# Kernel tuning notes

Hardware: AMD Instinct MI355X
Metric: run time of the kernel (lower is better)

The kernel has to match this reference:

```python
import jax, jax.numpy as jnp
import numpy as np

NUM_HEAD = 16
EMBD_DIM = 2048
LATENT_DIM = 512
ROPE_DIM = 64  # min(rope_dim, head_dim) = 64
HEAD_DIM = EMBD_DIM // NUM_HEAD  # 128
ROPE_HALF = ROPE_DIM // 2
SCALE = (HEAD_DIM + ROPE_DIM) ** -0.5


def setup_inputs() -> dict:
    key = jax.random.key(0)
    ks = jax.random.split(key, 9)
    B, S = 2, 2048
    std = 0.02
    return {
        "x": jax.random.normal(ks[0], (B, S, EMBD_DIM), dtype=jnp.float32),
        "w_ckv": jax.random.normal(ks[1], (EMBD_DIM, LATENT_DIM), dtype=jnp.float32) * std,
        "w_k": jax.random.normal(ks[2], (LATENT_DIM, EMBD_DIM), dtype=jnp.float32) * std,
        "w_v": jax.random.normal(ks[3], (LATENT_DIM, EMBD_DIM), dtype=jnp.float32) * std,
        "w_cq": jax.random.normal(ks[4], (EMBD_DIM, LATENT_DIM), dtype=jnp.float32) * std,
        "w_q": jax.random.normal(ks[5], (LATENT_DIM, EMBD_DIM), dtype=jnp.float32) * std,
        "w_qr": jax.random.normal(ks[6], (LATENT_DIM, NUM_HEAD * ROPE_DIM), dtype=jnp.float32) * std,
        "w_kr": jax.random.normal(ks[7], (EMBD_DIM, ROPE_DIM), dtype=jnp.float32) * std,
        "w_o": jax.random.normal(ks[8], (EMBD_DIM, EMBD_DIM), dtype=jnp.float32) * std,
    }


def _apply_rope(x, S):
    # x: [B, H, S, D] with D >= ROPE_DIM; interleaved even/odd rotation
    inv_freq = 1.0 / (10000.0 ** (jnp.arange(0, ROPE_DIM, 2, dtype=jnp.float32) / ROPE_DIM))
    pos = jnp.arange(S, dtype=jnp.float32)
    freqs = pos[:, None] * inv_freq[None, :]           # [S, ROPE_HALF]
    cos = jnp.cos(freqs)[None, None]                   # [1,1,S,ROPE_HALF]
    sin = jnp.sin(freqs)[None, None]
    x_rope, x_pass = x[..., :ROPE_DIM], x[..., ROPE_DIM:]
    x_even, x_odd = x_rope[..., 0::2], x_rope[..., 1::2]
    r_even = x_even * cos - x_odd * sin
    r_odd = x_even * sin + x_odd * cos
    rotated = jnp.stack([r_even, r_odd], axis=-1).reshape(x_rope.shape)
    return jnp.concatenate([rotated, x_pass], axis=-1) if x_pass.shape[-1] > 0 else rotated


def reference(x, w_ckv, w_k, w_v, w_cq, w_q, w_qr, w_kr, w_o):
    B, S, _ = x.shape
    c_kv = x @ w_ckv                                   # [B,S,latent]
    k_c = (c_kv @ w_k).reshape(B, S, NUM_HEAD, HEAD_DIM).transpose(0, 2, 1, 3)
    v = (c_kv @ w_v).reshape(B, S, NUM_HEAD, HEAD_DIM).transpose(0, 2, 1, 3)
    c_q = x @ w_cq
    q_c = (c_q @ w_q).reshape(B, S, NUM_HEAD, HEAD_DIM).transpose(0, 2, 1, 3)
    q_r = (c_q @ w_qr).reshape(B, S, NUM_HEAD, ROPE_DIM).transpose(0, 2, 1, 3)
    k_r = (x @ w_kr)[:, None, :, :]                    # [B,1,S,rope] shared across heads
    k_r = jnp.broadcast_to(k_r, (B, NUM_HEAD, S, ROPE_DIM))
    q_r = _apply_rope(q_r, S)
    k_r = _apply_rope(k_r, S)
    q = jnp.concatenate([q_c, q_r], axis=-1)           # [B,H,S,head+rope]
    k = jnp.concatenate([k_c, k_r], axis=-1)
    scores = jnp.einsum("bhsd,bhtd->bhst", q, k) * SCALE
    causal = jnp.tril(jnp.ones((S, S), dtype=bool))
    scores = jnp.where(causal[None, None], scores, -jnp.inf)
    attn = jax.nn.softmax(scores, axis=-1)
    out = jnp.einsum("bhst,bhtd->bhsd", attn, v)       # [B,H,S,head]
    out = out.transpose(0, 2, 1, 3).reshape(B, S, EMBD_DIM)
    return out @ w_o
```

## Files before the change

kernel.cpp:

```cpp
#include <hip/hip_runtime.h>


typedef unsigned short u16;
typedef __attribute__((ext_vector_type(8))) short s16x8;
typedef __attribute__((ext_vector_type(4))) float f32x4;
typedef __attribute__((ext_vector_type(8))) __bf16 bf16x8;
typedef __attribute__((ext_vector_type(4))) u16 u16x4;

#define S_LEN 2048
#define NH 16
#define HD 128
#define DQK 192
#define EMB 2048

#define GLOAD_LDS16(g, l)                                                      \
  __builtin_amdgcn_global_load_lds(                                            \
      (const __attribute__((address_space(1))) unsigned int*)(g),              \
      (__attribute__((address_space(3))) unsigned int*)(l), 16, 0, 0)

__device__ __forceinline__ u16 f2b(float f) {
  unsigned u = __builtin_bit_cast(unsigned, f);
  u += 0x7FFFu + ((u >> 16) & 1u);
  return (u16)(u >> 16);
}
__device__ __forceinline__ float b2f(u16 v) {
  unsigned u = ((unsigned)v) << 16;
  return __builtin_bit_cast(float, u);
}
__device__ __forceinline__ bf16x8 ld_bf8(const u16* p) {
  return __builtin_bit_cast(bf16x8, *(const s16x8*)p);
}

__device__ __forceinline__ void transpose_tile(const float* __restrict__ in,
                                               u16* __restrict__ out,
                                               int K, int N, int local, int t,
                                               u16* T ) {
  int nt = N >> 6;
  int n0 = (local % nt) * 64, k0 = (local / nt) * 64;
#pragma unroll
  for (int r = 0; r < 4; ++r) {
    int kl = (t >> 4) + r * 16, nl = (t & 15) * 4;
    f32x4 v = *(const f32x4*)(in + (size_t)(k0 + kl) * N + n0 + nl);
#pragma unroll
    for (int j = 0; j < 4; ++j) T[(nl + j) * 72 + kl] = f2b(v[j]);
  }
  __syncthreads();
#pragma unroll
  for (int r = 0; r < 2; ++r) {
    int chunk = t + r * 256, nr = chunk >> 3, kc = (chunk & 7) * 8;
    *(s16x8*)(out + (size_t)(n0 + nr) * K + k0 + kc) = *(const s16x8*)(&T[nr * 72 + kc]);
  }
}

__global__ __launch_bounds__(256) void prep_kernel(
    const float* __restrict__ xf, u16* __restrict__ XB,
    const float* __restrict__ wckvf, u16* __restrict__ WCKV_T,
    const float* __restrict__ wcqf,  u16* __restrict__ WCQ_T,
    const float* __restrict__ wkrf,  u16* __restrict__ WKR_T,
    const float* __restrict__ wkf,   u16* __restrict__ WK_T,
    const float* __restrict__ wvf,   u16* __restrict__ WV_T,
    const float* __restrict__ wqf,   u16* __restrict__ WQ_T,
    const float* __restrict__ wqrf,  u16* __restrict__ WQR_T,
    const float* __restrict__ wof,   u16* __restrict__ WO_T,
    float* __restrict__ cosT, float* __restrict__ sinT) {
  __shared__ u16 T[64 * 72];
  const int id = blockIdx.x, t = threadIdx.x;
  if (id < 8192) {
    int i = id * 256 + t;
    f32x4 v = *(const f32x4*)(xf + (size_t)i * 4);
    u16x4 o = { f2b(v[0]), f2b(v[1]), f2b(v[2]), f2b(v[3]) };
    *(u16x4*)(XB + (size_t)i * 4) = o;
  } else if (id < 8448)  { transpose_tile(wckvf, WCKV_T, 2048, 512,  id - 8192, t, T); }
  else if (id < 8704)    { transpose_tile(wcqf,  WCQ_T,  2048, 512,  id - 8448, t, T); }
  else if (id < 8736)    { transpose_tile(wkrf,  WKR_T,  2048, 64,   id - 8704, t, T); }
  else if (id < 8992)    { transpose_tile(wkf,   WK_T,   512,  2048, id - 8736, t, T); }
  else if (id < 9248)    { transpose_tile(wvf,   WV_T,   512,  2048, id - 8992, t, T); }
  else if (id < 9504)    { transpose_tile(wqf,   WQ_T,   512,  2048, id - 9248, t, T); }
  else if (id < 9632)    { transpose_tile(wqrf,  WQR_T,  512,  1024, id - 9504, t, T); }
  else if (id < 10656)   { transpose_tile(wof,   WO_T,   2048, 2048, id - 9632, t, T); }
  else {
    int i2 = (id - 10656) * 256 + t;
    int s = i2 >> 5, i = i2 & 31;
    float inv = exp2f(-(float)i * (13.287712379549449f / 32.0f));
    float ang = (float)s * inv;
    cosT[i2] = cosf(ang);
    sinT[i2] = sinf(ang);
  }
}

template<int MODE>
__global__ __launch_bounds__(256) void gemm_bt_kernel(const u16* __restrict__ A,
                                                      int lda,
                                                      const u16* __restrict__ BT,
                                                      void* __restrict__ C0,
                                                      void* __restrict__ C1,
                                                      void* __restrict__ C2,
                                                      void* __restrict__ C3,
                                                      int M, int N, int K,
                                                      int nx, float scale) {
  __shared__ __align__(16) u16 As[2][128 * 64];
  __shared__ __align__(16) u16 Bs[2][128 * 64];
  const int t = threadIdx.x;
  const int lane = t & 63, wid = t >> 6;
  const int wr = (wid >> 1) * 64, wc = (wid & 1) * 64;
  const int cpx = gridDim.x >> 3;
  int wg = blockIdx.x;
  wg = (wg & 7) * cpx + (wg >> 3);
  const int bn0 = (wg % nx) * 128;
  const int bm0 = (wg / nx) * 128;
  if (MODE == 6 && bn0 >= 4096) A += 512;
  const int lr = lane & 15, lg = lane >> 4;

  auto stage = [&](int k0, int buf) {
#pragma unroll
    for (int r = 0; r < 4; ++r) {
      int chunk = t + r * 256;
      int row = chunk >> 3, kcs = (chunk & 7) * 8;
      int kcg = kcs ^ ((row & 7) << 3);
      GLOAD_LDS16(A + (size_t)(bm0 + row) * lda + k0 + kcg, &As[buf][chunk * 8]);
      GLOAD_LDS16(BT + (size_t)(bn0 + row) * K + k0 + kcg, &Bs[buf][chunk * 8]);
    }
  };

  f32x4 acc[4][4] = {};
  const int nt = K >> 6;
  stage(0, 0);
  for (int tk = 0; tk < nt; ++tk) {
    const int cur = tk & 1;
    __syncthreads();
    if (tk + 1 < nt) stage((tk + 1) << 6, cur ^ 1);
#pragma unroll
    for (int kk = 0; kk < 2; ++kk) {
      bf16x8 af[4], bfr[4];
      const int kbase = kk * 32 + lg * 8;
#pragma unroll
      for (int m = 0; m < 4; ++m) {
        int row = wr + m * 16 + lr;
        af[m] = ld_bf8(&As[cur][row * 64 + (kbase ^ ((row & 7) << 3))]);
      }
#pragma unroll
      for (int n = 0; n < 4; ++n) {
        int row = wc + n * 16 + lr;
        bfr[n] = ld_bf8(&Bs[cur][row * 64 + (kbase ^ ((row & 7) << 3))]);
      }
#pragma unroll
      for (int m = 0; m < 4; ++m)
#pragma unroll
        for (int n = 0; n < 4; ++n)
          acc[m][n] = __builtin_amdgcn_mfma_f32_16x16x32_bf16(af[m], bfr[n], acc[m][n], 0, 0, 0);
    }
  }

#pragma unroll
  for (int m = 0; m < 4; ++m)
#pragma unroll
    for (int n = 0; n < 4; ++n)
#pragma unroll
      for (int rg = 0; rg < 4; ++rg) {
        int row = bm0 + wr + m * 16 + lg * 4 + rg;
        int col = bn0 + wc + n * 16 + lr;
        if (col >= N) continue;
        float v = acc[m][n][rg];
        if (MODE == 0) {
          ((u16*)C0)[(size_t)row * N + col] = f2b(v * scale);
        } else if (MODE == 1) {
          ((float*)C0)[(size_t)row * N + col] = v * scale;
        } else {
          int bb = row >> 11, s = row & 2047;
          if (col < 2048) {
            int h = col >> 7, d = col & 127;
            ((u16*)C0)[((size_t)(bb * NH + h) * S_LEN + s) * DQK + d] = f2b(v);
          } else if (col < 4096) {
            int c2 = col - 2048, h = c2 >> 7, d = c2 & 127;
            ((u16*)C1)[((size_t)(bb * NH + h) * HD + d) * S_LEN + s] = f2b(v);
          } else if (col < 6144) {
            int c3 = col - 4096, h = c3 >> 7, d = c3 & 127;
            ((u16*)C2)[((size_t)(bb * NH + h) * S_LEN + s) * DQK + d] = f2b(v * scale);
          } else {
            ((u16*)C3)[(size_t)row * 1024 + (col - 6144)] = f2b(v);
          }
        }
      }
}

__global__ __launch_bounds__(256) void rope_assemble_kernel(const u16* __restrict__ qr,
                                                            const u16* __restrict__ cc,
                                                            const float* __restrict__ cosT,
                                                            const float* __restrict__ sinT,
                                                            u16* __restrict__ Qcat,
                                                            u16* __restrict__ Kcat) {
  int id = blockIdx.x * 256 + threadIdx.x;
  int i = id & 31;
  int s = (id >> 5) & 2047;
  int h = (id >> 16) & 15;
  int b = id >> 20;
  float c = cosT[(s << 5) + i], sn = sinT[(s << 5) + i];
  const float SC = 0.07216878364870323f * 1.4426950408889634f;

  size_t qbase = ((size_t)b * S_LEN + s) * 1024 + h * 64 + 2 * i;
  float qe = b2f(qr[qbase]), qo = b2f(qr[qbase + 1]);
  size_t obase = ((size_t)(b * NH + h) * S_LEN + s) * DQK + HD + 2 * i;
  Qcat[obase]     = f2b((qe * c - qo * sn) * SC);
  Qcat[obase + 1] = f2b((qe * sn + qo * c) * SC);

  size_t kbase = ((size_t)b * S_LEN + s) * 1088 + 1024 + 2 * i;
  float ke = b2f(cc[kbase]), ko = b2f(cc[kbase + 1]);
  Kcat[obase]     = f2b(ke * c - ko * sn);
  Kcat[obase + 1] = f2b(ke * sn + ko * c);
}

__global__ __launch_bounds__(512, 2) void attn_kernel(const u16* __restrict__ Q,
                                                      const u16* __restrict__ K,
                                                      const u16* __restrict__ VT,
                                                      u16* __restrict__ O) {
  __shared__ u16 Ks[64 * 200];
  __shared__ u16 Vs[128 * 72];
  __shared__ u16 Ps[8 * 16 * 88];
  const int id = blockIdx.x;
  const int p8 = id >> 5, hb = id & 31;
  const int h = hb & 15, b = hb >> 4;
  const int qb = (p8 < 8) ? p8 : 23 - p8;
  const int q0 = qb * 128;
  const int t = threadIdx.x, lane = t & 63, wid = t >> 6;
  const int lr = lane & 15, lg = lane >> 4;
  const size_t qk_head = (size_t)(b * NH + h) * S_LEN * DQK;
  const size_t vt_head = (size_t)(b * NH + h) * HD * S_LEN;

  s16x8 kst[3], vst[2];
  auto gload = [&](int kt) {
#pragma unroll
    for (int r = 0; r < 3; ++r) {
      int chunk = t + r * 512, row = chunk / 24, cc = chunk % 24;
      kst[r] = *(const s16x8*)(K + qk_head + (size_t)(kt * 64 + row) * DQK + cc * 8);
    }
#pragma unroll
    for (int r = 0; r < 2; ++r) {
      int chunk = t + r * 512, d = chunk >> 3, cc = chunk & 7;
      vst[r] = *(const s16x8*)(VT + vt_head + (size_t)d * S_LEN + kt * 64 + cc * 8);
    }
  };
  auto swr = [&]() {
#pragma unroll
    for (int r = 0; r < 3; ++r) {
      int chunk = t + r * 512, row = chunk / 24, cc = chunk % 24;
      *(s16x8*)(&Ks[row * 200 + cc * 8]) = kst[r];
    }
#pragma unroll
    for (int r = 0; r < 2; ++r) {
      int chunk = t + r * 512, d = chunk >> 3, cc = chunk & 7;
      *(s16x8*)(&Vs[d * 72 + cc * 8]) = vst[r];
    }
  };

  bf16x8 qa[6];
  {
    const u16* qrow = Q + qk_head + (size_t)(q0 + wid * 16 + lr) * DQK;
#pragma unroll
    for (int ks = 0; ks < 6; ++ks) qa[ks] = ld_bf8(qrow + ks * 32 + lg * 8);
  }

  f32x4 acc_o[8] = {};
  float m_r[4] = { -INFINITY, -INFINITY, -INFINITY, -INFINITY };
  float l_r[4] = { 0.f, 0.f, 0.f, 0.f };

  const int nt = 2 * qb + 2;
  gload(0);
#pragma unroll 1
  for (int kt = 0; kt < nt; ++kt) {
    __syncthreads();
    swr();
    __syncthreads();
    if (kt + 1 < nt) gload(kt + 1);

    f32x4 sacc[4];
#pragma unroll
    for (int cb = 0; cb < 4; ++cb) {
      f32x4 sv = {};
#pragma unroll
      for (int ks = 0; ks < 6; ++ks) {
        bf16x8 kb = ld_bf8(&Ks[(cb * 16 + lr) * 200 + ks * 32 + lg * 8]);
        sv = __builtin_amdgcn_mfma_f32_16x16x32_bf16(qa[ks], kb, sv, 0, 0, 0);
      }
      sacc[cb] = sv;
    }

    if (kt >= 2 * qb) {
#pragma unroll
      for (int cb = 0; cb < 4; ++cb)
#pragma unroll
        for (int rg = 0; rg < 4; ++rg) {
          int q_g = q0 + wid * 16 + lg * 4 + rg;
          int kv_g = kt * 64 + cb * 16 + lr;
          if (kv_g > q_g) sacc[cb][rg] = -INFINITY;
        }
    }

    float pmax[4];
#pragma unroll
    for (int rg = 0; rg < 4; ++rg)
      pmax[rg] = fmaxf(fmaxf(sacc[0][rg], sacc[1][rg]), fmaxf(sacc[2][rg], sacc[3][rg]));
#pragma unroll
    for (int off = 1; off < 16; off <<= 1)
#pragma unroll
      for (int rg = 0; rg < 4; ++rg)
        pmax[rg] = fmaxf(pmax[rg], __shfl_xor(pmax[rg], off, 64));

    int nochange = (pmax[0] <= m_r[0] + 8.f) & (pmax[1] <= m_r[1] + 8.f) &
                   (pmax[2] <= m_r[2] + 8.f) & (pmax[3] <= m_r[3] + 8.f);
    if (!__all(nochange)) {
      float alpha[4];
#pragma unroll
      for (int rg = 0; rg < 4; ++rg) {
        float mn = fmaxf(m_r[rg], pmax[rg]);
        alpha[rg] = exp2f(m_r[rg] - mn);
        m_r[rg] = mn;
        l_r[rg] *= alpha[rg];
      }
#pragma unroll
      for (int vb = 0; vb < 8; ++vb)
#pragma unroll
        for (int rg = 0; rg < 4; ++rg)
          acc_o[vb][rg] *= alpha[rg];
    }

    float psum[4] = { 0.f, 0.f, 0.f, 0.f };
#pragma unroll
    for (int cb = 0; cb < 4; ++cb)
#pragma unroll
      for (int rg = 0; rg < 4; ++rg) {
        float pv = exp2f(sacc[cb][rg] - m_r[rg]);
        sacc[cb][rg] = pv;
        psum[rg] += pv;
      }
#pragma unroll
    for (int off = 1; off < 16; off <<= 1)
#pragma unroll
      for (int rg = 0; rg < 4; ++rg)
        psum[rg] += __shfl_xor(psum[rg], off, 64);
#pragma unroll
    for (int rg = 0; rg < 4; ++rg) l_r[rg] += psum[rg];

    u16* psw = &Ps[wid * (16 * 88)];
#pragma unroll
    for (int cb = 0; cb < 4; ++cb)
#pragma unroll
      for (int rg = 0; rg < 4; ++rg)
        psw[(lg * 4 + rg) * 88 + cb * 16 + lr] = f2b(sacc[cb][rg]);

    bf16x8 pa[2];
#pragma unroll
    for (int ks = 0; ks < 2; ++ks) pa[ks] = ld_bf8(&psw[lr * 88 + ks * 32 + lg * 8]);
#pragma unroll
    for (int vb = 0; vb < 8; ++vb) {
#pragma unroll
      for (int ks = 0; ks < 2; ++ks) {
        bf16x8 vv = ld_bf8(&Vs[(vb * 16 + lr) * 72 + ks * 32 + lg * 8]);
        acc_o[vb] = __builtin_amdgcn_mfma_f32_16x16x32_bf16(pa[ks], vv, acc_o[vb], 0, 0, 0);
      }
    }
  }

#pragma unroll
  for (int vb = 0; vb < 8; ++vb)
#pragma unroll
    for (int rg = 0; rg < 4; ++rg) {
      int s_glob = q0 + wid * 16 + lg * 4 + rg;
      int col = vb * 16 + lr;
      O[((size_t)b * S_LEN + s_glob) * EMB + h * HD + col] = f2b(acc_o[vb][rg] / l_r[rg]);
    }
}

extern "C" void kernel_launch(void* const* d_in, const int* in_sizes, int n_in,
                              void* d_out, int out_size, void* d_ws, size_t ws_size,
                              hipStream_t stream) {
  const float* xf    = (const float*)d_in[0];
  const float* wckvf = (const float*)d_in[1];
  const float* wkf   = (const float*)d_in[2];
  const float* wvf   = (const float*)d_in[3];
  const float* wcqf  = (const float*)d_in[4];
  const float* wqf   = (const float*)d_in[5];
  const float* wqrf  = (const float*)d_in[6];
  const float* wkrf  = (const float*)d_in[7];
  const float* wof   = (const float*)d_in[8];
  (void)in_sizes; (void)n_in; (void)out_size; (void)ws_size;

  u16* ws = (u16*)d_ws;
  size_t off = 0;
  auto alloc = [&](size_t n) -> u16* { u16* p = ws + off; off += n; return p; };
  u16* XB     = alloc(8388608);
  u16* WCKV_T = alloc(1048576);
  u16* WCQ_T  = alloc(1048576);
  u16* WKR_T  = alloc(131072);
  u16* WK_T   = alloc(1048576);
  u16* WV_T   = alloc(1048576);
  u16* WQ_T   = alloc(1048576);
  u16* WQR_T  = alloc(524288);
  u16* WO_T   = alloc(4194304);
  u16* CC     = alloc(4456448);
  u16* QR     = alloc(4194304);
  u16* QCAT   = alloc(12582912);
  u16* KCAT   = alloc(12582912);
  u16* VT     = alloc(8388608);
  u16* AOUT   = alloc(8388608);
  float* COS_T = (float*)alloc(131072);
  float* SIN_T = (float*)alloc(131072);

  prep_kernel<<<10912, 256, 0, stream>>>(xf, XB,
                                         wckvf, WCKV_T, wcqf, WCQ_T, wkrf, WKR_T,
                                         wkf, WK_T, wvf, WV_T, wqf, WQ_T,
                                         wqrf, WQR_T, wof, WO_T,
                                         COS_T, SIN_T);

  const float SC = 0.07216878364870323f * 1.4426950408889634f;
  gemm_bt_kernel<0><<<288, 256, 0, stream>>>(XB, 2048, WCKV_T, CC,
                                             nullptr, nullptr, nullptr,
                                             4096, 1088, 2048, 9, 1.0f);
  gemm_bt_kernel<6><<<1792, 256, 0, stream>>>(CC, 1088, WK_T, KCAT, VT, QCAT, QR,
                                              4096, 7168, 512, 56, SC);

  rope_assemble_kernel<<<8192, 256, 0, stream>>>(QR, CC, COS_T, SIN_T, QCAT, KCAT);

  attn_kernel<<<512, 512, 0, stream>>>(QCAT, KCAT, VT, AOUT);

  gemm_bt_kernel<1><<<512, 256, 0, stream>>>(AOUT, 2048, WO_T, d_out,
                                             nullptr, nullptr, nullptr,
                                             4096, 2048, 2048, 16, 1.0f);
}
```

Measured before the change: 275.3 us.

## Fuse RoPE into GEMM epilogues and drop the separate rope kernel

Applies the rotary embedding inside the GEMM epilogues. Pairs come from a lane shuffle, q-rope is written straight into QCAT and k-rope is broadcast to all 16 heads of KCAT. This removes the rope_assemble launch and the QR round trip through global memory. The ckv GEMM epilogue now does 16 scattered stores per rope column. The attention loop also issues the next tile's global loads before the second barrier rather than after it, to overlap them with the barrier wait.

Result: slower. 625.2 us (+127.1%).

```diff
diff --git a/kernel.cpp b/kernel.cpp
--- a/kernel.cpp
+++ b/kernel.cpp
@@ -95,7 +95,8 @@
                                                       void* __restrict__ C0,
                                                       void* __restrict__ C1,
                                                       void* __restrict__ C2,
-                                                      void* __restrict__ C3,
+                                                      const float* __restrict__ cosT,
+                                                      const float* __restrict__ sinT,
                                                       int M, int N, int K,
                                                       int nx, float scale) {
   __shared__ __align__(16) u16 As[2][128 * 64];
@@ -159,12 +160,23 @@
       for (int rg = 0; rg < 4; ++rg) {
         int row = bm0 + wr + m * 16 + lg * 4 + rg;
         int col = bn0 + wc + n * 16 + lr;
+        float v = acc[m][n][rg];
+        float p = (MODE == 6 || MODE == 7) ? __shfl_xor(v, 1, 64) : 0.f;
         if (col >= N) continue;
-        float v = acc[m][n][rg];
-        if (MODE == 0) {
-          ((u16*)C0)[(size_t)row * N + col] = f2b(v * scale);
-        } else if (MODE == 1) {
+        if (MODE == 1) {
           ((float*)C0)[(size_t)row * N + col] = v * scale;
+        } else if (MODE == 7) {
+          if (col < 1024) {
+            ((u16*)C0)[(size_t)row * 1088 + col] = f2b(v);
+          } else {
+            int s = row & 2047, bb = row >> 11, d = col & 63, i = d >> 1;
+            float c = cosT[(s << 5) + i], sn = sinT[(s << 5) + i];
+            float out = ((lr & 1) == 0) ? (v * c - p * sn) : (p * sn + v * c);
+            u16 o = f2b(out);
+#pragma unroll
+            for (int hh = 0; hh < 16; ++hh)
+              ((u16*)C1)[((size_t)(bb * NH + hh) * S_LEN + s) * DQK + HD + d] = o;
+          }
         } else {
           int bb = row >> 11, s = row & 2047;
           if (col < 2048) {
@@ -177,36 +189,13 @@
             int c3 = col - 4096, h = c3 >> 7, d = c3 & 127;
             ((u16*)C2)[((size_t)(bb * NH + h) * S_LEN + s) * DQK + d] = f2b(v * scale);
           } else {
-            ((u16*)C3)[(size_t)row * 1024 + (col - 6144)] = f2b(v);
+            int dd = col - 6144, h = dd >> 6, d = dd & 63, i = d >> 1;
+            float c = cosT[(s << 5) + i], sn = sinT[(s << 5) + i];
+            float out = (((lr & 1) == 0) ? (v * c - p * sn) : (p * sn + v * c)) * scale;
+            ((u16*)C2)[((size_t)(bb * NH + h) * S_LEN + s) * DQK + HD + d] = f2b(out);
           }
         }
       }
-}
-
-__global__ __launch_bounds__(256) void rope_assemble_kernel(const u16* __restrict__ qr,
-                                                            const u16* __restrict__ cc,
-                                                            const float* __restrict__ cosT,
-                                                            const float* __restrict__ sinT,
-                                                            u16* __restrict__ Qcat,
-                                                            u16* __restrict__ Kcat) {
-  int id = blockIdx.x * 256 + threadIdx.x;
-  int i = id & 31;
-  int s = (id >> 5) & 2047;
-  int h = (id >> 16) & 15;
-  int b = id >> 20;
-  float c = cosT[(s << 5) + i], sn = sinT[(s << 5) + i];
-  const float SC = 0.07216878364870323f * 1.4426950408889634f;
-
-  size_t qbase = ((size_t)b * S_LEN + s) * 1024 + h * 64 + 2 * i;
-  float qe = b2f(qr[qbase]), qo = b2f(qr[qbase + 1]);
-  size_t obase = ((size_t)(b * NH + h) * S_LEN + s) * DQK + HD + 2 * i;
-  Qcat[obase]     = f2b((qe * c - qo * sn) * SC);
-  Qcat[obase + 1] = f2b((qe * sn + qo * c) * SC);
-
-  size_t kbase = ((size_t)b * S_LEN + s) * 1088 + 1024 + 2 * i;
-  float ke = b2f(cc[kbase]), ko = b2f(cc[kbase + 1]);
-  Kcat[obase]     = f2b(ke * c - ko * sn);
-  Kcat[obase + 1] = f2b(ke * sn + ko * c);
 }
 
 __global__ __launch_bounds__(512, 2) void attn_kernel(const u16* __restrict__ Q,
@@ -269,8 +258,8 @@
   for (int kt = 0; kt < nt; ++kt) {
     __syncthreads();
     swr();
+    if (kt + 1 < nt) gload(kt + 1);
     __syncthreads();
-    if (kt + 1 < nt) gload(kt + 1);
 
     f32x4 sacc[4];
 #pragma unroll
@@ -397,7 +386,6 @@
   u16* WQR_T  = alloc(524288);
   u16* WO_T   = alloc(4194304);
   u16* CC     = alloc(4456448);
-  u16* QR     = alloc(4194304);
   u16* QCAT   = alloc(12582912);
   u16* KCAT   = alloc(12582912);
   u16* VT     = alloc(8388608);
@@ -412,17 +400,17 @@
                                          COS_T, SIN_T);
 
   const float SC = 0.07216878364870323f * 1.4426950408889634f;
-  gemm_bt_kernel<0><<<288, 256, 0, stream>>>(XB, 2048, WCKV_T, CC,
-                                             nullptr, nullptr, nullptr,
+  gemm_bt_kernel<7><<<288, 256, 0, stream>>>(XB, 2048, WCKV_T, CC, KCAT, nullptr,
+                                             COS_T, SIN_T,
                                              4096, 1088, 2048, 9, 1.0f);
-  gemm_bt_kernel<6><<<1792, 256, 0, stream>>>(CC, 1088, WK_T, KCAT, VT, QCAT, QR,
+  gemm_bt_kernel<6><<<1792, 256, 0, stream>>>(CC, 1088, WK_T, KCAT, VT, QCAT,
+                                              COS_T, SIN_T,
                                               4096, 7168, 512, 56, SC);
 
-  rope_assemble_kernel<<<8192, 256, 0, stream>>>(QR, CC, COS_T, SIN_T, QCAT, KCAT);
-
   attn_kernel<<<512, 512, 0, stream>>>(QCAT, KCAT, VT, AOUT);
 
   gemm_bt_kernel<1><<<512, 256, 0, stream>>>(AOUT, 2048, WO_T, d_out,
-                                             nullptr, nullptr, nullptr,
+                                             nullptr, nullptr,
+                                             nullptr, nullptr,
                                              4096, 2048, 2048, 16, 1.0f);
 }
```
